# Kernel optimization log

Hardware: AMD Instinct MI355X
Metric: run time of the kernel (lower is better)

The kernel has to match this reference:

```python
import jax, jax.numpy as jnp
import numpy as np

N_NODES = 50000
N_EDGES = 800000
D_IN = 64   # input_dimension + 1
D_HID = 64


def _gcn_conv(x, src, dst, W, b, deg_isqrt):
    # PyG GCNConv: X' = D^{-1/2} (A + I) D^{-1/2} X W + b
    h = x @ W  # [N, H]
    norm = (deg_isqrt[src] * deg_isqrt[dst])[:, None]  # [E, 1]
    agg = jax.ops.segment_sum(h[src] * norm, dst, num_segments=x.shape[0])
    # self-loop contribution: norm_ii = deg_isqrt[i]^2
    agg = agg + h * (deg_isqrt * deg_isqrt)[:, None]
    return agg + b


def setup_inputs() -> dict:
    key = jax.random.key(0)
    ks = jax.random.split(key, 8)
    x = jax.random.normal(ks[0], (N_NODES, D_IN), dtype=jnp.float32)
    edge_index = jax.random.randint(ks[1], (2, N_EDGES), 0, N_NODES, dtype=jnp.int32)
    s = 1.0 / np.sqrt(D_HID)
    W0 = jax.random.normal(ks[2], (D_IN, D_HID), dtype=jnp.float32) * s
    b0 = jnp.zeros((D_HID,), dtype=jnp.float32)
    W1 = jax.random.normal(ks[3], (D_HID, D_HID), dtype=jnp.float32) * s
    b1 = jnp.zeros((D_HID,), dtype=jnp.float32)
    W2 = jax.random.normal(ks[4], (D_HID, D_HID), dtype=jnp.float32) * s
    b2 = jnp.zeros((D_HID,), dtype=jnp.float32)
    Wout = jax.random.normal(ks[5], (D_HID, 1), dtype=jnp.float32) * s
    bout = jnp.zeros((1,), dtype=jnp.float32)
    return {"x": x, "edge_index": edge_index, "W0": W0, "b0": b0,
            "W1": W1, "b1": b1, "W2": W2, "b2": b2,
            "Wout": Wout, "bout": bout}


def reference(x, edge_index, W0, b0, W1, b1, W2, b2, Wout, bout):
    src, dst = edge_index[0], edge_index[1]
    n = x.shape[0]
    # degree with self-loop (edge weight 1.0 each)
    deg = jnp.zeros((n,), x.dtype).at[dst].add(1.0) + 1.0
    deg_isqrt = jax.lax.rsqrt(deg)
    h = jax.nn.relu(_gcn_conv(x, src, dst, W0, b0, deg_isqrt))
    h = jax.nn.relu(_gcn_conv(h, src, dst, W1, b1, deg_isqrt))
    h = jax.nn.relu(_gcn_conv(h, src, dst, W2, b2, deg_isqrt))
    return h @ Wout + bout  # [N, 1]
```

## Files before the change

### kernel.cpp

```cpp
#include <hip/hip_runtime.h>
#include <hip/hip_bf16.h>

#define D 64
#define N_NODES 50000
#define N_EDGES 800000

__global__ void zero_i(int* __restrict__ p, int n) {
    int i = blockIdx.x * blockDim.x + threadIdx.x;
    if (i < n) p[i] = 0;
}

__global__ void hist_k(const int* __restrict__ dst, int* __restrict__ cnt, int E) {
    int i = blockIdx.x * blockDim.x + threadIdx.x;
    if (i < E) atomicAdd(&cnt[dst[i]], 1);
}

__global__ void dis_k(const int* __restrict__ cnt, float* __restrict__ dis, int n) {
    int i = blockIdx.x * blockDim.x + threadIdx.x;
    if (i < n) dis[i] = rsqrtf((float)cnt[i] + 1.0f);
}

__global__ void scan1_k(const int* __restrict__ cnt, int* __restrict__ off,
                        int* __restrict__ bsum, int N) {
    __shared__ int sh[256];
    int t = threadIdx.x;
    int i = blockIdx.x * 256 + t;
    int v = (i < N) ? cnt[i] : 0;
    sh[t] = v;
    __syncthreads();
#pragma unroll
    for (int d = 1; d < 256; d <<= 1) {
        int u = (t >= d) ? sh[t - d] : 0;
        __syncthreads();
        sh[t] += u;
        __syncthreads();
    }
    if (i < N) off[i] = sh[t] - v;
    if (t == 255) bsum[blockIdx.x] = sh[255];
}

__global__ void scan2_k(int* __restrict__ bsum, int nb) {
    __shared__ int sh[256];
    int t = threadIdx.x;
    int v = (t < nb) ? bsum[t] : 0;
    sh[t] = v;
    __syncthreads();
#pragma unroll
    for (int d = 1; d < 256; d <<= 1) {
        int u = (t >= d) ? sh[t - d] : 0;
        __syncthreads();
        sh[t] += u;
        __syncthreads();
    }
    if (t < nb) bsum[t] = sh[t] - v;
}

__global__ void scan3_k(int* __restrict__ off, const int* __restrict__ bsum,
                        int* __restrict__ cursor, int N, int E) {
    int i = blockIdx.x * 256 + threadIdx.x;
    if (i < N) {
        int o = off[i] + bsum[blockIdx.x];
        off[i] = o;
        cursor[i] = o;
    }
    if (i == 0) off[N] = E;
}

__global__ void fill_k(const int* __restrict__ src, const int* __restrict__ dst,
                       int* __restrict__ cursor, int* __restrict__ esrc, int E) {
    int i = blockIdx.x * blockDim.x + threadIdx.x;
    if (i < E) {
        int pos = atomicAdd(&cursor[dst[i]], 1);
        esrc[pos] = src[i];
    }
}

template <int PRE>
__global__ void gemm_k(const float* __restrict__ X, const float* __restrict__ W,
                       const float* __restrict__ dis, const float* __restrict__ bias,
                       float* __restrict__ H, int N) {
    __shared__ float Ws[D * D];
    __shared__ float Xs[4][D];
    for (int i = threadIdx.x; i < D * D; i += blockDim.x) Ws[i] = W[i];
    __syncthreads();

    int r = threadIdx.x >> 6;
    int c = threadIdx.x & 63;

    for (int row0 = blockIdx.x * 4; row0 < N; row0 += gridDim.x * 4) {
        int row = row0 + r;
        if (row < N) {
            float v = X[(size_t)row * D + c];
            if (PRE == 1) v = fmaxf(fmaf(v, dis[row], bias[c]), 0.0f);
            Xs[r][c] = v;
        }
        __syncthreads();
        if (row < N) {
            float acc = 0.0f;
#pragma unroll
            for (int k = 0; k < D; ++k) acc = fmaf(Xs[r][k], Ws[k * D + c], acc);
            H[(size_t)row * D + c] = acc * dis[row];
        }
        __syncthreads();
    }
}

__global__ void agg_k(const float4* __restrict__ Hs4, const int* __restrict__ off,
                      const int* __restrict__ esrc, float4* __restrict__ AGG4, int N) {
    int wid = (blockIdx.x * blockDim.x + threadIdx.x) >> 6;
    int lane = threadIdx.x & 63;
    if (wid >= N) return;
    int grp = lane >> 4;
    int l16 = lane & 15;
    int beg = off[wid], end = off[wid + 1];

    float4 acc = make_float4(0.f, 0.f, 0.f, 0.f);
    if (grp == 0) acc = Hs4[(size_t)wid * 16 + l16];

    for (int j = beg + grp; j < end; j += 4) {
        int s = esrc[j];
        float4 v = Hs4[(size_t)s * 16 + l16];
        acc.x += v.x; acc.y += v.y; acc.z += v.z; acc.w += v.w;
    }
#pragma unroll
    for (int m = 16; m <= 32; m <<= 1) {
        acc.x += __shfl_xor(acc.x, m, 64);
        acc.y += __shfl_xor(acc.y, m, 64);
        acc.z += __shfl_xor(acc.z, m, 64);
        acc.w += __shfl_xor(acc.w, m, 64);
    }
    if (grp == 0) AGG4[(size_t)wid * 16 + l16] = acc;
}

__global__ void proj_k(const float* __restrict__ AGG, const float* __restrict__ dis,
                       const float* __restrict__ bias, const float* __restrict__ Wout,
                       const float* __restrict__ bout, float* __restrict__ out, int N) {
    int wid = (blockIdx.x * blockDim.x + threadIdx.x) >> 6;
    int lane = threadIdx.x & 63;
    if (wid >= N) return;
    float wc = Wout[lane];
    float b = bout[0];
    float v = fmaxf(fmaf(AGG[(size_t)wid * D + lane], dis[wid], bias[lane]), 0.0f) * wc;
#pragma unroll
    for (int off = 32; off; off >>= 1) v += __shfl_down(v, off, 64);
    if (lane == 0) out[wid] = v + b;
}

extern "C" void kernel_launch(void* const* d_in, const int* in_sizes, int n_in,
                              void* d_out, int out_size, void* d_ws, size_t ws_size,
                              hipStream_t stream) {
    const float* x    = (const float*)d_in[0];
    const int*   ei   = (const int*)d_in[1];
    const float* W0   = (const float*)d_in[2];
    const float* b0   = (const float*)d_in[3];
    const float* W1   = (const float*)d_in[4];
    const float* b1   = (const float*)d_in[5];
    const float* W2   = (const float*)d_in[6];
    const float* b2   = (const float*)d_in[7];
    const float* Wout = (const float*)d_in[8];
    const float* bout = (const float*)d_in[9];
    float* out = (float*)d_out;

    const int N = N_NODES, E = N_EDGES;
    const int* src = ei;
    const int* dst = ei + E;

    char* ws = (char*)d_ws;
    int*   cnt    = (int*)(ws);
    int*   off    = (int*)(ws + (256u << 10));
    int*   cursor = (int*)(ws + (512u << 10));
    float* dis    = (float*)(ws + (768u << 10));
    int*   bsum   = (int*)(ws + (990u << 10));
    int*   esrc   = (int*)(ws + (1u << 20));
    float* bufA   = (float*)(ws + (5u << 20));
    float* bufB   = (float*)(ws + (18u << 20));

    dim3 blk(256);
    const int NB = (N + 255) / 256;
    dim3 gN(NB);
    dim3 gE((E + 255) / 256);
    dim3 gAgg((N * 64 + 255) / 256);
    dim3 gGemm(2048);

    zero_i<<<gN, blk, 0, stream>>>(cnt, N);
    hist_k<<<gE, blk, 0, stream>>>(dst, cnt, E);
    dis_k<<<gN, blk, 0, stream>>>(cnt, dis, N);
    scan1_k<<<gN, blk, 0, stream>>>(cnt, off, bsum, N);
    scan2_k<<<1, blk, 0, stream>>>(bsum, NB);
    scan3_k<<<gN, blk, 0, stream>>>(off, bsum, cursor, N, E);
    fill_k<<<gE, blk, 0, stream>>>(src, dst, cursor, esrc, E);

    gemm_k<0><<<gGemm, blk, 0, stream>>>(x, W0, dis, nullptr, bufA, N);
    agg_k<<<gAgg, blk, 0, stream>>>((const float4*)bufA, off, esrc, (float4*)bufB, N);

    gemm_k<1><<<gGemm, blk, 0, stream>>>(bufB, W1, dis, b0, bufA, N);
    agg_k<<<gAgg, blk, 0, stream>>>((const float4*)bufA, off, esrc, (float4*)bufB, N);

    gemm_k<1><<<gGemm, blk, 0, stream>>>(bufB, W2, dis, b1, bufA, N);
    agg_k<<<gAgg, blk, 0, stream>>>((const float4*)bufA, off, esrc, (float4*)bufB, N);

    proj_k<<<gAgg, blk, 0, stream>>>(bufB, dis, b2, Wout, bout, out, N);
}
```

Baseline: 353.9 us.

## Fuse aggregation with next-layer GEMM and overlap CSR fill with first GEMM

```diff
diff --git a/kernel.cpp b/kernel.cpp
--- a/kernel.cpp
+++ b/kernel.cpp
@@ -5,23 +5,13 @@
 #define N_NODES 50000
 #define N_EDGES 800000
 
-__global__ void zero_i(int* __restrict__ p, int n) {
-    int i = blockIdx.x * blockDim.x + threadIdx.x;
-    if (i < n) p[i] = 0;
-}
-
 __global__ void hist_k(const int* __restrict__ dst, int* __restrict__ cnt, int E) {
     int i = blockIdx.x * blockDim.x + threadIdx.x;
     if (i < E) atomicAdd(&cnt[dst[i]], 1);
 }
 
-__global__ void dis_k(const int* __restrict__ cnt, float* __restrict__ dis, int n) {
-    int i = blockIdx.x * blockDim.x + threadIdx.x;
-    if (i < n) dis[i] = rsqrtf((float)cnt[i] + 1.0f);
-}
-
 __global__ void scan1_k(const int* __restrict__ cnt, int* __restrict__ off,
-                        int* __restrict__ bsum, int N) {
+                        int* __restrict__ bsum, float* __restrict__ dis, int N) {
     __shared__ int sh[256];
     int t = threadIdx.x;
     int i = blockIdx.x * 256 + t;
@@ -35,7 +25,10 @@
         sh[t] += u;
         __syncthreads();
     }
-    if (i < N) off[i] = sh[t] - v;
+    if (i < N) {
+        off[i] = sh[t] - v;
+        dis[i] = rsqrtf((float)v + 1.0f);
+    }
     if (t == 255) bsum[blockIdx.x] = sh[255];
 }
 
@@ -66,58 +59,78 @@
     if (i == 0) off[N] = E;
 }
 
-__global__ void fill_k(const int* __restrict__ src, const int* __restrict__ dst,
-                       int* __restrict__ cursor, int* __restrict__ esrc, int E) {
-    int i = blockIdx.x * blockDim.x + threadIdx.x;
-    if (i < E) {
-        int pos = atomicAdd(&cursor[dst[i]], 1);
-        esrc[pos] = src[i];
-    }
-}
-
-template <int PRE>
-__global__ void gemm_k(const float* __restrict__ X, const float* __restrict__ W,
-                       const float* __restrict__ dis, const float* __restrict__ bias,
-                       float* __restrict__ H, int N) {
+__global__ void fused0_k(const float* __restrict__ X, const float* __restrict__ W,
+                         const float* __restrict__ dis, float* __restrict__ H,
+                         const int* __restrict__ src, const int* __restrict__ dst,
+                         int* __restrict__ cursor, int* __restrict__ esrc,
+                         int N, int E, int gemmBlocks) {
     __shared__ float Ws[D * D];
     __shared__ float Xs[4][D];
-    for (int i = threadIdx.x; i < D * D; i += blockDim.x) Ws[i] = W[i];
-    __syncthreads();
-
-    int r = threadIdx.x >> 6;
-    int c = threadIdx.x & 63;
-
-    for (int row0 = blockIdx.x * 4; row0 < N; row0 += gridDim.x * 4) {
-        int row = row0 + r;
-        if (row < N) {
-            float v = X[(size_t)row * D + c];
-            if (PRE == 1) v = fmaxf(fmaf(v, dis[row], bias[c]), 0.0f);
-            Xs[r][c] = v;
+    int bid = blockIdx.x;
+    if (bid < gemmBlocks) {
+        for (int i = threadIdx.x; i < D * D; i += blockDim.x) Ws[i] = W[i];
+        __syncthreads();
+        int r = threadIdx.x >> 6;
+        int c = threadIdx.x & 63;
+        for (int row0 = bid * 4; row0 < N; row0 += gemmBlocks * 4) {
+            int row = row0 + r;
+            if (row < N) Xs[r][c] = X[(size_t)row * D + c];
+            __syncthreads();
+            if (row < N) {
+                float acc = 0.0f;
+#pragma unroll
+                for (int k = 0; k < D; ++k) acc = fmaf(Xs[r][k], Ws[k * D + c], acc);
+                H[(size_t)row * D + c] = acc * dis[row];
+            }
+            __syncthreads();
         }
-        __syncthreads();
-        if (row < N) {
-            float acc = 0.0f;
-#pragma unroll
-            for (int k = 0; k < D; ++k) acc = fmaf(Xs[r][k], Ws[k * D + c], acc);
-            H[(size_t)row * D + c] = acc * dis[row];
+    } else {
+        int fb = bid - gemmBlocks;
+        int nfb = gridDim.x - gemmBlocks;
+        for (int i = fb * 256 + threadIdx.x; i < E; i += nfb * 256) {
+            int pos = atomicAdd(&cursor[dst[i]], 1);
+            esrc[pos] = src[i];
         }
-        __syncthreads();
-    }
-}
-
-__global__ void agg_k(const float4* __restrict__ Hs4, const int* __restrict__ off,
-                      const int* __restrict__ esrc, float4* __restrict__ AGG4, int N) {
+    }
+}
+
+template <int FINAL>
+__global__ void layer_k(const float4* __restrict__ Hs4, const int* __restrict__ off,
+                        const int* __restrict__ esrc, const float* __restrict__ dis,
+                        const float* __restrict__ bias, const float* __restrict__ W,
+                        const float* __restrict__ bout, float* __restrict__ outp, int N) {
     int wid = (blockIdx.x * blockDim.x + threadIdx.x) >> 6;
     int lane = threadIdx.x & 63;
-    if (wid >= N) return;
     int grp = lane >> 4;
     int l16 = lane & 15;
+    int c = lane;
+
+    float Wc[64];
+    if (!FINAL) {
+#pragma unroll
+        for (int k = 0; k < 64; ++k) Wc[k] = W[k * 64 + c];
+    }
+    float4 b4 = ((const float4*)bias)[l16];
+
+    if (wid >= N) return;
+
     int beg = off[wid], end = off[wid + 1];
-
     float4 acc = make_float4(0.f, 0.f, 0.f, 0.f);
     if (grp == 0) acc = Hs4[(size_t)wid * 16 + l16];
 
-    for (int j = beg + grp; j < end; j += 4) {
+    int j = beg + grp;
+    for (; j + 12 < end; j += 16) {
+        int s0 = esrc[j], s1 = esrc[j + 4], s2 = esrc[j + 8], s3 = esrc[j + 12];
+        float4 v0 = Hs4[(size_t)s0 * 16 + l16];
+        float4 v1 = Hs4[(size_t)s1 * 16 + l16];
+        float4 v2 = Hs4[(size_t)s2 * 16 + l16];
+        float4 v3 = Hs4[(size_t)s3 * 16 + l16];
+        acc.x += (v0.x + v1.x) + (v2.x + v3.x);
+        acc.y += (v0.y + v1.y) + (v2.y + v3.y);
+        acc.z += (v0.z + v1.z) + (v2.z + v3.z);
+        acc.w += (v0.w + v1.w) + (v2.w + v3.w);
+    }
+    for (; j < end; j += 4) {
         int s = esrc[j];
         float4 v = Hs4[(size_t)s * 16 + l16];
         acc.x += v.x; acc.y += v.y; acc.z += v.z; acc.w += v.w;
@@ -129,21 +142,36 @@
         acc.z += __shfl_xor(acc.z, m, 64);
         acc.w += __shfl_xor(acc.w, m, 64);
     }
-    if (grp == 0) AGG4[(size_t)wid * 16 + l16] = acc;
-}
-
-__global__ void proj_k(const float* __restrict__ AGG, const float* __restrict__ dis,
-                       const float* __restrict__ bias, const float* __restrict__ Wout,
-                       const float* __restrict__ bout, float* __restrict__ out, int N) {
-    int wid = (blockIdx.x * blockDim.x + threadIdx.x) >> 6;
-    int lane = threadIdx.x & 63;
-    if (wid >= N) return;
-    float wc = Wout[lane];
-    float b = bout[0];
-    float v = fmaxf(fmaf(AGG[(size_t)wid * D + lane], dis[wid], bias[lane]), 0.0f) * wc;
-#pragma unroll
-    for (int off = 32; off; off >>= 1) v += __shfl_down(v, off, 64);
-    if (lane == 0) out[wid] = v + b;
+    float dv = dis[wid];
+    float4 h4;
+    h4.x = fmaxf(fmaf(acc.x, dv, b4.x), 0.f);
+    h4.y = fmaxf(fmaf(acc.y, dv, b4.y), 0.f);
+    h4.z = fmaxf(fmaf(acc.z, dv, b4.z), 0.f);
+    h4.w = fmaxf(fmaf(acc.w, dv, b4.w), 0.f);
+
+    if (FINAL) {
+        float4 w4 = ((const float4*)W)[l16];
+        float p = h4.x * w4.x + h4.y * w4.y + h4.z * w4.z + h4.w * w4.w;
+        p += __shfl_xor(p, 1, 64);
+        p += __shfl_xor(p, 2, 64);
+        p += __shfl_xor(p, 4, 64);
+        p += __shfl_xor(p, 8, 64);
+        if (lane == 0) outp[wid] = p + bout[0];
+    } else {
+        float o = 0.f;
+#pragma unroll
+        for (int ch = 0; ch < 16; ++ch) {
+            float hx = __shfl(h4.x, ch, 64);
+            float hy = __shfl(h4.y, ch, 64);
+            float hz = __shfl(h4.z, ch, 64);
+            float hw = __shfl(h4.w, ch, 64);
+            o = fmaf(hx, Wc[4 * ch + 0], o);
+            o = fmaf(hy, Wc[4 * ch + 1], o);
+            o = fmaf(hz, Wc[4 * ch + 2], o);
+            o = fmaf(hw, Wc[4 * ch + 3], o);
+        }
+        outp[(size_t)wid * 64 + c] = o * dv;
+    }
 }
 
 extern "C" void kernel_launch(void* const* d_in, const int* in_sizes, int n_in,
@@ -179,25 +207,23 @@
     const int NB = (N + 255) / 256;
     dim3 gN(NB);
     dim3 gE((E + 255) / 256);
-    dim3 gAgg((N * 64 + 255) / 256);
-    dim3 gGemm(2048);
-
-    zero_i<<<gN, blk, 0, stream>>>(cnt, N);
+    dim3 gWave((N * 64 + 255) / 256);
+    const int GEMM_BLOCKS = 2048;
+    const int FILL_BLOCKS = 1024;
+
+    hipMemsetAsync(cnt, 0, (size_t)N * sizeof(int), stream);
     hist_k<<<gE, blk, 0, stream>>>(dst, cnt, E);
-    dis_k<<<gN, blk, 0, stream>>>(cnt, dis, N);
-    scan1_k<<<gN, blk, 0, stream>>>(cnt, off, bsum, N);
+    scan1_k<<<gN, blk, 0, stream>>>(cnt, off, bsum, dis, N);
     scan2_k<<<1, blk, 0, stream>>>(bsum, NB);
     scan3_k<<<gN, blk, 0, stream>>>(off, bsum, cursor, N, E);
-    fill_k<<<gE, blk, 0, stream>>>(src, dst, cursor, esrc, E);
-
-    gemm_k<0><<<gGemm, blk, 0, stream>>>(x, W0, dis, nullptr, bufA, N);
-    agg_k<<<gAgg, blk, 0, stream>>>((const float4*)bufA, off, esrc, (float4*)bufB, N);
-
-    gemm_k<1><<<gGemm, blk, 0, stream>>>(bufB, W1, dis, b0, bufA, N);
-    agg_k<<<gAgg, blk, 0, stream>>>((const float4*)bufA, off, esrc, (float4*)bufB, N);
-
-    gemm_k<1><<<gGemm, blk, 0, stream>>>(bufB, W2, dis, b1, bufA, N);
-    agg_k<<<gAgg, blk, 0, stream>>>((const float4*)bufA, off, esrc, (float4*)bufB, N);
-
-    proj_k<<<gAgg, blk, 0, stream>>>(bufB, dis, b2, Wout, bout, out, N);
-}
+
+    fused0_k<<<dim3(GEMM_BLOCKS + FILL_BLOCKS), blk, 0, stream>>>(
+        x, W0, dis, bufA, src, dst, cursor, esrc, N, E, GEMM_BLOCKS);
+
+    layer_k<0><<<gWave, blk, 0, stream>>>((const float4*)bufA, off, esrc, dis,
+                                          b0, W1, nullptr, bufB, N);
+    layer_k<0><<<gWave, blk, 0, stream>>>((const float4*)bufB, off, esrc, dis,
+                                          b1, W2, nullptr, bufA, N);
+    layer_k<1><<<gWave, blk, 0, stream>>>((const float4*)bufA, off, esrc, dis,
+                                          b2, Wout, bout, out, N);
+}
```

After: 345.9 us. 2.3% less time.
